# Kernel tuning notes

Hardware: AMD Instinct MI355X
Metric: run time of the kernel (lower is better)

The kernel has to match this reference:

```python
import jax, jax.numpy as jnp
import numpy as np

D_MODEL = 1024
NUM_HEADS = 16
D_K = D_MODEL // NUM_HEADS
B, S = 4, 2048


def setup_inputs() -> dict:
    key = jax.random.key(0)
    k1, k2, k3 = jax.random.split(key, 3)
    x = jax.random.normal(k1, (B, S, D_MODEL), dtype=jnp.float32)
    w_qkv = jax.random.normal(k2, (3, NUM_HEADS, D_K, D_MODEL), dtype=jnp.float32) / np.sqrt(D_MODEL)
    w_o = jax.random.normal(k3, (D_MODEL, D_MODEL), dtype=jnp.float32) / np.sqrt(D_MODEL)
    return {"x": x, "w_qkv": w_qkv, "w_o": w_o}


def reference(x, w_qkv, w_o):
    # x: [b, s, m]; w_qkv: [3, h, k, m]; w_o: [m, m]
    seq_len = x.shape[-2]
    d_k = w_qkv.shape[-2]
    # fused QKV projection for all heads: [3, b, h, s, k]
    qkv = jnp.einsum('bsm,qhkm->qbhsk', x, w_qkv)
    Q, K, V = qkv[0], qkv[1], qkv[2]
    # attention scores [b, h, s, s]
    scores = jnp.einsum('bhsk,bhtk->bhst', Q, K) / jnp.sqrt(jnp.asarray(d_k, x.dtype))
    # causal mask: position t > s is masked
    causal = jnp.tril(jnp.ones((seq_len, seq_len), dtype=bool))
    scores = jnp.where(causal, scores, -jnp.inf)
    probs = jax.nn.softmax(scores, axis=-1)
    # attn_pdrop = 0.0 -> dropout is identity
    attn = jnp.einsum('bhst,bhtk->bhsk', probs, V)
    # concat heads: [b, s, h*k]
    b, h, s, k = attn.shape
    attn_cat = jnp.transpose(attn, (0, 2, 1, 3)).reshape(b, s, h * k)
    # output projection: y = attn_cat @ w_o^T
    return jnp.einsum('bsd,md->bsm', attn_cat, w_o)
```

## Files before the change

### kernel.cpp

```cpp
#include <hip/hip_runtime.h>
#include <hip/hip_bf16.h>


#define D_MODEL 1024
#define NUM_HEADS 16
#define D_KD 64
#define B_SZ 4
#define S_LEN 2048
#define ROWS (B_SZ * S_LEN)
#define QKV_N (3 * D_MODEL)

typedef __attribute__((ext_vector_type(8))) short short8;
typedef __attribute__((ext_vector_type(4))) float f32x4;
typedef __attribute__((ext_vector_type(16))) float f32x16;

__device__ __forceinline__ unsigned f2bf(float f) {
    unsigned u = __builtin_bit_cast(unsigned, f);
    return (u + 0x7FFFu + ((u >> 16) & 1u)) >> 16;
}
__device__ __forceinline__ uint2 pack_bf16x4(float4 v) {
    uint2 u;
    u.x = f2bf(v.x) | (f2bf(v.y) << 16);
    u.y = f2bf(v.z) | (f2bf(v.w) << 16);
    return u;
}

template <int MODE>
__global__ __launch_bounds__(256) void gemm_bt_mfma(const float* __restrict__ A,
                                                    const float* __restrict__ Bm,
                                                    float* __restrict__ C,
                                                    int M, int N, int K) {
    __shared__ unsigned short As[128][40];
    __shared__ unsigned short Bs[128][40];

    const int t = threadIdx.x;
    const int lane = t & 63;
    const int w = t >> 6;
    const int wr = w >> 1, wc = w & 1;
    const int row0 = blockIdx.y * 128;
    const int col0 = blockIdx.x * 128;

    const int srow = t >> 3;
    const int skc = (t & 7) << 2;

    const float* Abase = A + (size_t)row0 * K;
    const float* Bbase = Bm + (size_t)col0 * K;

    f32x4 acc[4][4];
#pragma unroll
    for (int m = 0; m < 4; ++m)
#pragma unroll
        for (int n = 0; n < 4; ++n)
#pragma unroll
            for (int j = 0; j < 4; ++j) acc[m][n][j] = 0.f;

    float4 pa[4], pb[4];
    const int q8 = (lane >> 4) << 3;
    const int frA = wr * 64 + (lane & 15);
    const int frB = wc * 64 + (lane & 15);
    const int NT = K >> 5;

#pragma unroll
    for (int i = 0; i < 4; ++i) {
        int r = i * 32 + srow;
        pa[i] = *reinterpret_cast<const float4*>(&Abase[(size_t)r * K + skc]);
        pb[i] = *reinterpret_cast<const float4*>(&Bbase[(size_t)r * K + skc]);
    }

    for (int kt = 0; kt < NT; ++kt) {
        __syncthreads();
#pragma unroll
        for (int i = 0; i < 4; ++i) {
            int r = i * 32 + srow;
            *reinterpret_cast<uint2*>(&As[r][skc]) = pack_bf16x4(pa[i]);
            *reinterpret_cast<uint2*>(&Bs[r][skc]) = pack_bf16x4(pb[i]);
        }
        __syncthreads();

        if (kt + 1 < NT) {
            const int k0n = (kt + 1) << 5;
#pragma unroll
            for (int i = 0; i < 4; ++i) {
                int r = i * 32 + srow;
                pa[i] = *reinterpret_cast<const float4*>(&Abase[(size_t)r * K + k0n + skc]);
                pb[i] = *reinterpret_cast<const float4*>(&Bbase[(size_t)r * K + k0n + skc]);
            }
        }

        short8 afr[4], bfr[4];
#pragma unroll
        for (int m = 0; m < 4; ++m)
            afr[m] = *reinterpret_cast<const short8*>(&As[frA + m * 16][q8]);
#pragma unroll
        for (int n = 0; n < 4; ++n)
            bfr[n] = *reinterpret_cast<const short8*>(&Bs[frB + n * 16][q8]);
#pragma unroll
        for (int m = 0; m < 4; ++m)
#pragma unroll
            for (int n = 0; n < 4; ++n)
                acc[m][n] = __builtin_amdgcn_mfma_f32_16x16x32_bf16(afr[m], bfr[n],
                                                                    acc[m][n], 0, 0, 0);
    }

    const int orow = row0 + wr * 64 + ((lane >> 4) << 2);
    const int ocol = col0 + wc * 64 + (lane & 15);
#pragma unroll
    for (int m = 0; m < 4; ++m)
#pragma unroll
        for (int n = 0; n < 4; ++n) {
            const int cg = ocol + n * 16;
#pragma unroll
            for (int j = 0; j < 4; ++j) {
                const int rg = orow + m * 16 + j;
                const float v = acc[m][n][j];
                if (MODE == 0) {
                    int q = cg >> 10, h = (cg >> 6) & 15, kk = cg & 63;
                    int b = rg >> 11, s = rg & 2047;
                    C[((((size_t)q * B_SZ + b) * NUM_HEADS + h) * S_LEN + s) * D_KD + kk] = v;
                } else {
                    C[(size_t)rg * N + cg] = v;
                }
            }
        }
}

__global__ __launch_bounds__(512, 2) void flash_attn_mfma_v2(const float* __restrict__ qkv,
                                                             float* __restrict__ attn_out) {
    const int qb = (int)gridDim.x - 1 - (int)blockIdx.x;
    const int h = blockIdx.y;
    const int b = blockIdx.z;
    const int t = threadIdx.x;
    const int lane = t & 63;
    const int w = t >> 6;
    const int l31 = lane & 31;
    const int hi = lane >> 5;

    __shared__ unsigned short smem[256 * 72];
    __shared__ float fbuf[8][32];

    unsigned short* Qs = smem;
    unsigned short* Ks = smem;
    unsigned short* Vt = smem + 64 * 72;

    const size_t head_elems = (size_t)S_LEN * D_KD;
    const float* Qg = qkv + (((size_t)0 * B_SZ + b) * NUM_HEADS + h) * head_elems;
    const float* Kg = qkv + (((size_t)1 * B_SZ + b) * NUM_HEADS + h) * head_elems;
    const float* Vg = qkv + (((size_t)2 * B_SZ + b) * NUM_HEADS + h) * head_elems;

    const int q0 = qb * 256;
    const int qmin = q0 + 32 * w;

#pragma unroll
    for (int lx = 0; lx < 8; ++lx) {
        int idx = t + lx * 512;
        int r = idx >> 4;
        int c = (idx & 15) << 2;
        float4 v = *reinterpret_cast<const float4*>(&Qg[(size_t)(q0 + r) * D_KD + c]);
        v.x *= 0.125f; v.y *= 0.125f; v.z *= 0.125f; v.w *= 0.125f;
        *reinterpret_cast<uint2*>(&Qs[r * 72 + c]) = pack_bf16x4(v);
    }
    __syncthreads();

    short8 qfr[4];
#pragma unroll
    for (int ks = 0; ks < 4; ++ks)
        qfr[ks] = *reinterpret_cast<const short8*>(&Qs[(32 * w + l31) * 72 + 16 * ks + 8 * hi]);

    f32x16 oacc[2];
#pragma unroll
    for (int n = 0; n < 2; ++n)
#pragma unroll
        for (int j = 0; j < 16; ++j) oacc[n][j] = 0.f;
    float m = -1e30f, lsum = 0.f;

    const int nt = 4 * (qb + 1);
    for (int tt = 0; tt < nt; ++tt) {
        const int c0 = tt * 64;
        __syncthreads();

        if (w < 4) {
#pragma unroll
            for (int lx = 0; lx < 4; ++lx) {
                int idx = t + lx * 256;
                int r = idx >> 4;
                int c = (idx & 15) << 2;
                float4 v = *reinterpret_cast<const float4*>(&Kg[(size_t)(c0 + r) * D_KD + c]);
                *reinterpret_cast<uint2*>(&Ks[r * 72 + c]) = pack_bf16x4(v);
            }
        } else {
            int t2 = t - 256;
            int tb = (t2 >> 4) << 2;
            int dk0 = (t2 & 15) << 2;
            float4 vv[4];
#pragma unroll
            for (int i = 0; i < 4; ++i)
                vv[i] = *reinterpret_cast<const float4*>(&Vg[(size_t)(c0 + tb + i) * D_KD + dk0]);
            const float* vp = reinterpret_cast<const float*>(&vv[0]);
#pragma unroll
            for (int j = 0; j < 4; ++j) {
                uint2 u;
                u.x = f2bf(vp[0 * 4 + j]) | (f2bf(vp[1 * 4 + j]) << 16);
                u.y = f2bf(vp[2 * 4 + j]) | (f2bf(vp[3 * 4 + j]) << 16);
                *reinterpret_cast<uint2*>(&Vt[(dk0 + j) * 72 + tb]) = u;
            }
        }
        __syncthreads();

        for (int st = 0; st < 2; ++st) {
            const int t0s = c0 + 32 * st;
            if (t0s > qmin) break;
            const bool diag = (t0s == qmin);

            f32x16 s;
#pragma unroll
            for (int j = 0; j < 16; ++j) s[j] = 0.f;
#pragma unroll
            for (int ks = 0; ks < 4; ++ks) {
                short8 ka = *reinterpret_cast<const short8*>(
                    &Ks[(32 * st + l31) * 72 + 16 * ks + 8 * hi]);
                s = __builtin_amdgcn_mfma_f32_32x32x16_bf16(ka, qfr[ks], s, 0, 0, 0);
            }
            if (diag) {
#pragma unroll
                for (int reg = 0; reg < 16; ++reg) {
                    const int tloc = (reg & 3) + 8 * (reg >> 2) + 4 * hi;
                    if (tloc > l31) s[reg] = -1e30f;
                }
            }

            float pm = s[0];
#pragma unroll
            for (int reg = 1; reg < 16; ++reg) pm = fmaxf(pm, s[reg]);
            pm = fmaxf(pm, __shfl_xor(pm, 32));

            if (!__all(pm <= m + 8.0f)) {
                const float mnew = fmaxf(m, pm);
                const float al = __expf(m - mnew);
                m = mnew;
                lsum *= al;
                fbuf[w][l31] = al;
#pragma unroll
                for (int g = 0; g < 4; ++g) {
                    float4 a4 = *reinterpret_cast<float4*>(&fbuf[w][8 * g + 4 * hi]);
                    const float* ap = reinterpret_cast<const float*>(&a4);
#pragma unroll
                    for (int j = 0; j < 4; ++j) {
                        oacc[0][4 * g + j] *= ap[j];
                        oacc[1][4 * g + j] *= ap[j];
                    }
                }
            }

            float p[16];
            float ps = 0.f;
#pragma unroll
            for (int reg = 0; reg < 16; ++reg) {
                p[reg] = __expf(s[reg] - m);
                ps += p[reg];
            }
            ps += __shfl_xor(ps, 32);
            lsum += ps;

            unsigned pk[8], sw[8];
#pragma unroll
            for (int i = 0; i < 8; ++i) pk[i] = f2bf(p[2 * i]) | (f2bf(p[2 * i + 1]) << 16);
#pragma unroll
            for (int i = 0; i < 8; ++i) sw[i] = (unsigned)__shfl_xor((int)pk[i], 32);

            union { unsigned u[4]; short8 s8; } a0, a1;
            a0.u[0] = hi ? sw[2] : pk[0];
            a0.u[1] = hi ? sw[3] : pk[1];
            a0.u[2] = hi ? pk[2] : sw[0];
            a0.u[3] = hi ? pk[3] : sw[1];
            a1.u[0] = hi ? sw[6] : pk[4];
            a1.u[1] = hi ? sw[7] : pk[5];
            a1.u[2] = hi ? pk[6] : sw[4];
            a1.u[3] = hi ? pk[7] : sw[5];

#pragma unroll
            for (int n = 0; n < 2; ++n) {
                const unsigned short* vrow = &Vt[(32 * n + l31) * 72 + 32 * st + 8 * hi];
                short8 vb0 = *reinterpret_cast<const short8*>(vrow);
                short8 vb1 = *reinterpret_cast<const short8*>(vrow + 16);
                oacc[n] = __builtin_amdgcn_mfma_f32_32x32x16_bf16(a0.s8, vb0, oacc[n], 0, 0, 0);
                oacc[n] = __builtin_amdgcn_mfma_f32_32x32x16_bf16(a1.s8, vb1, oacc[n], 0, 0, 0);
            }
        }
    }

    const float inv = 1.f / lsum;
    fbuf[w][l31] = inv;
#pragma unroll
    for (int g = 0; g < 4; ++g) {
        float4 i4 = *reinterpret_cast<float4*>(&fbuf[w][8 * g + 4 * hi]);
        const float* ip = reinterpret_cast<const float*>(&i4);
#pragma unroll
        for (int j = 0; j < 4; ++j) {
            const int reg = 4 * g + j;
            const int qrow = q0 + 32 * w + 8 * g + 4 * hi + j;
            const size_t base = ((size_t)(b * S_LEN + qrow)) * D_MODEL + h * D_KD + l31;
            attn_out[base] = oacc[0][reg] * ip[j];
            attn_out[base + 32] = oacc[1][reg] * ip[j];
        }
    }
}

extern "C" void kernel_launch(void* const* d_in, const int* in_sizes, int n_in,
                              void* d_out, int out_size, void* d_ws, size_t ws_size,
                              hipStream_t stream) {
    const float* x = (const float*)d_in[0];
    const float* w_qkv = (const float*)d_in[1];
    const float* w_o = (const float*)d_in[2];
    float* out = (float*)d_out;

    float* qkv = (float*)d_ws;
    float* attn = qkv + (size_t)3 * B_SZ * NUM_HEADS * S_LEN * D_KD;

    gemm_bt_mfma<0><<<dim3(QKV_N / 128, ROWS / 128), dim3(256), 0, stream>>>(
        x, w_qkv, qkv, ROWS, QKV_N, D_MODEL);
    flash_attn_mfma_v2<<<dim3(S_LEN / 256, NUM_HEADS, B_SZ), dim3(512), 0, stream>>>(qkv, attn);
    gemm_bt_mfma<1><<<dim3(D_MODEL / 128, ROWS / 128), dim3(256), 0, stream>>>(
        attn, w_o, out, ROWS, D_MODEL, D_MODEL);
}
```

Baseline: 364.3 us.

## Switch pipeline to bf16 intermediates with pre-converted inputs and direct-to-LDS GEMM loads

Three small kernels first convert x, w_qkv and w_o to bf16. The QKV GEMM then writes bf16 Q/K/V, with the 1/sqrt(d_k) scale folded into its epilogue, and attention writes a bf16 attention output. This halves intermediate traffic and removes per-tile float-to-bf16 conversion inside the attention and GEMM loops. The GEMM now loads tiles with global_load_lds into unpadded shared memory, which drops the register prefetch overlap and may add LDS bank conflicts. The attention MFMA sections are also wrapped in s_setprio to favour matrix issue.

```diff
diff --git a/kernel.cpp b/kernel.cpp
--- a/kernel.cpp
+++ b/kernel.cpp
@@ -13,6 +13,7 @@
 typedef __attribute__((ext_vector_type(8))) short short8;
 typedef __attribute__((ext_vector_type(4))) float f32x4;
 typedef __attribute__((ext_vector_type(16))) float f32x16;
+typedef unsigned short ushort_t;
 
 __device__ __forceinline__ unsigned f2bf(float f) {
     unsigned u = __builtin_bit_cast(unsigned, f);
@@ -24,14 +25,30 @@
     u.y = f2bf(v.z) | (f2bf(v.w) << 16);
     return u;
 }
+__device__ __forceinline__ void gload16(void* lds, const void* g) {
+    __builtin_amdgcn_global_load_lds(
+        (const __attribute__((address_space(1))) unsigned int*)(g),
+        (__attribute__((address_space(3))) unsigned int*)(lds), 16, 0, 0);
+}
+
+__global__ __launch_bounds__(256) void cvt_bf16(const float* __restrict__ src,
+                                                ushort_t* __restrict__ dst, int n4) {
+    int i = blockIdx.x * blockDim.x + threadIdx.x;
+    const int stride = gridDim.x * blockDim.x;
+    for (; i < n4; i += stride) {
+        float4 v = reinterpret_cast<const float4*>(src)[i];
+        *reinterpret_cast<uint2*>(&dst[(size_t)i * 4]) = pack_bf16x4(v);
+    }
+}
 
 template <int MODE>
-__global__ __launch_bounds__(256) void gemm_bt_mfma(const float* __restrict__ A,
-                                                    const float* __restrict__ Bm,
-                                                    float* __restrict__ C,
+__global__ __launch_bounds__(256) void gemm_bt_bf16(const ushort_t* __restrict__ A,
+                                                    const ushort_t* __restrict__ Bm,
+                                                    ushort_t* __restrict__ Cb,
+                                                    float* __restrict__ Cf,
                                                     int M, int N, int K) {
-    __shared__ unsigned short As[128][40];
-    __shared__ unsigned short Bs[128][40];
+    __shared__ ushort_t As[128 * 32];
+    __shared__ ushort_t Bs[128 * 32];
 
     const int t = threadIdx.x;
     const int lane = t & 63;
@@ -40,11 +57,15 @@
     const int row0 = blockIdx.y * 128;
     const int col0 = blockIdx.x * 128;
 
-    const int srow = t >> 3;
-    const int skc = (t & 7) << 2;
-
-    const float* Abase = A + (size_t)row0 * K;
-    const float* Bbase = Bm + (size_t)col0 * K;
+    const int srow = t >> 2;
+    const int sk8 = (t & 3) << 3;
+
+    const ushort_t* Ag = A + (size_t)(row0 + srow) * K + sk8;
+    const ushort_t* Bg = Bm + (size_t)(col0 + srow) * K + sk8;
+    ushort_t* ldsA0 = &As[(size_t)t * 8];
+    ushort_t* ldsA1 = &As[(size_t)(t + 256) * 8];
+    ushort_t* ldsB0 = &Bs[(size_t)t * 8];
+    ushort_t* ldsB1 = &Bs[(size_t)(t + 256) * 8];
 
     f32x4 acc[4][4];
 #pragma unroll
@@ -54,46 +75,27 @@
 #pragma unroll
             for (int j = 0; j < 4; ++j) acc[m][n][j] = 0.f;
 
-    float4 pa[4], pb[4];
     const int q8 = (lane >> 4) << 3;
     const int frA = wr * 64 + (lane & 15);
     const int frB = wc * 64 + (lane & 15);
     const int NT = K >> 5;
 
-#pragma unroll
-    for (int i = 0; i < 4; ++i) {
-        int r = i * 32 + srow;
-        pa[i] = *reinterpret_cast<const float4*>(&Abase[(size_t)r * K + skc]);
-        pb[i] = *reinterpret_cast<const float4*>(&Bbase[(size_t)r * K + skc]);
-    }
-
     for (int kt = 0; kt < NT; ++kt) {
+        const int k0 = kt << 5;
         __syncthreads();
-#pragma unroll
-        for (int i = 0; i < 4; ++i) {
-            int r = i * 32 + srow;
-            *reinterpret_cast<uint2*>(&As[r][skc]) = pack_bf16x4(pa[i]);
-            *reinterpret_cast<uint2*>(&Bs[r][skc]) = pack_bf16x4(pb[i]);
-        }
+        gload16(ldsA0, Ag + k0);
+        gload16(ldsA1, Ag + (size_t)64 * K + k0);
+        gload16(ldsB0, Bg + k0);
+        gload16(ldsB1, Bg + (size_t)64 * K + k0);
         __syncthreads();
 
-        if (kt + 1 < NT) {
-            const int k0n = (kt + 1) << 5;
-#pragma unroll
-            for (int i = 0; i < 4; ++i) {
-                int r = i * 32 + srow;
-                pa[i] = *reinterpret_cast<const float4*>(&Abase[(size_t)r * K + k0n + skc]);
-                pb[i] = *reinterpret_cast<const float4*>(&Bbase[(size_t)r * K + k0n + skc]);
-            }
-        }
-
         short8 afr[4], bfr[4];
 #pragma unroll
         for (int m = 0; m < 4; ++m)
-            afr[m] = *reinterpret_cast<const short8*>(&As[frA + m * 16][q8]);
+            afr[m] = *reinterpret_cast<const short8*>(&As[(frA + m * 16) * 32 + q8]);
 #pragma unroll
         for (int n = 0; n < 4; ++n)
-            bfr[n] = *reinterpret_cast<const short8*>(&Bs[frB + n * 16][q8]);
+            bfr[n] = *reinterpret_cast<const short8*>(&Bs[(frB + n * 16) * 32 + q8]);
 #pragma unroll
         for (int m = 0; m < 4; ++m)
 #pragma unroll
@@ -112,20 +114,22 @@
 #pragma unroll
             for (int j = 0; j < 4; ++j) {
                 const int rg = orow + m * 16 + j;
-                const float v = acc[m][n][j];
+                float v = acc[m][n][j];
                 if (MODE == 0) {
-                    int q = cg >> 10, h = (cg >> 6) & 15, kk = cg & 63;
-                    int b = rg >> 11, s = rg & 2047;
-                    C[((((size_t)q * B_SZ + b) * NUM_HEADS + h) * S_LEN + s) * D_KD + kk] = v;
+                    const int q = cg >> 10, hh = (cg >> 6) & 15, kk = cg & 63;
+                    const int bb = rg >> 11, s = rg & 2047;
+                    if (q == 0) v *= 0.125f;
+                    Cb[((((size_t)q * B_SZ + bb) * NUM_HEADS + hh) * S_LEN + s) * D_KD + kk] =
+                        (ushort_t)f2bf(v);
                 } else {
-                    C[(size_t)rg * N + cg] = v;
+                    Cf[(size_t)rg * N + cg] = v;
                 }
             }
         }
 }
 
-__global__ __launch_bounds__(512, 2) void flash_attn_mfma_v2(const float* __restrict__ qkv,
-                                                             float* __restrict__ attn_out) {
+__global__ __launch_bounds__(512, 2) void flash_attn_mfma_v3(const ushort_t* __restrict__ qkv,
+                                                             ushort_t* __restrict__ attn_out) {
     const int qb = (int)gridDim.x - 1 - (int)blockIdx.x;
     const int h = blockIdx.y;
     const int b = blockIdx.z;
@@ -135,29 +139,27 @@
     const int l31 = lane & 31;
     const int hi = lane >> 5;
 
-    __shared__ unsigned short smem[256 * 72];
+    __shared__ ushort_t smem[256 * 72];
     __shared__ float fbuf[8][32];
-
-    unsigned short* Qs = smem;
-    unsigned short* Ks = smem;
-    unsigned short* Vt = smem + 64 * 72;
+    ushort_t* Qs = smem;
+    ushort_t* Ks = smem;
+    ushort_t* Vt = smem + 64 * 72;
 
     const size_t head_elems = (size_t)S_LEN * D_KD;
-    const float* Qg = qkv + (((size_t)0 * B_SZ + b) * NUM_HEADS + h) * head_elems;
-    const float* Kg = qkv + (((size_t)1 * B_SZ + b) * NUM_HEADS + h) * head_elems;
-    const float* Vg = qkv + (((size_t)2 * B_SZ + b) * NUM_HEADS + h) * head_elems;
+    const ushort_t* Qg = qkv + (((size_t)0 * B_SZ + b) * NUM_HEADS + h) * head_elems;
+    const ushort_t* Kg = qkv + (((size_t)1 * B_SZ + b) * NUM_HEADS + h) * head_elems;
+    const ushort_t* Vg = qkv + (((size_t)2 * B_SZ + b) * NUM_HEADS + h) * head_elems;
 
     const int q0 = qb * 256;
     const int qmin = q0 + 32 * w;
 
 #pragma unroll
-    for (int lx = 0; lx < 8; ++lx) {
+    for (int lx = 0; lx < 4; ++lx) {
         int idx = t + lx * 512;
-        int r = idx >> 4;
-        int c = (idx & 15) << 2;
-        float4 v = *reinterpret_cast<const float4*>(&Qg[(size_t)(q0 + r) * D_KD + c]);
-        v.x *= 0.125f; v.y *= 0.125f; v.z *= 0.125f; v.w *= 0.125f;
-        *reinterpret_cast<uint2*>(&Qs[r * 72 + c]) = pack_bf16x4(v);
+        int r = idx >> 3;
+        int c8 = (idx & 7) << 3;
+        *reinterpret_cast<uint4*>(&Qs[r * 72 + c8]) =
+            *reinterpret_cast<const uint4*>(&Qg[(size_t)(q0 + r) * D_KD + c8]);
     }
     __syncthreads();
 
@@ -180,28 +182,25 @@
 
         if (w < 4) {
 #pragma unroll
-            for (int lx = 0; lx < 4; ++lx) {
-                int idx = t + lx * 256;
-                int r = idx >> 4;
-                int c = (idx & 15) << 2;
-                float4 v = *reinterpret_cast<const float4*>(&Kg[(size_t)(c0 + r) * D_KD + c]);
-                *reinterpret_cast<uint2*>(&Ks[r * 72 + c]) = pack_bf16x4(v);
+            for (int i = 0; i < 2; ++i) {
+                int j = t + i * 256;
+                int r = j >> 3;
+                int c8 = (j & 7) << 3;
+                *reinterpret_cast<uint4*>(&Ks[r * 72 + c8]) =
+                    *reinterpret_cast<const uint4*>(&Kg[(size_t)(c0 + r) * D_KD + c8]);
             }
         } else {
             int t2 = t - 256;
-            int tb = (t2 >> 4) << 2;
-            int dk0 = (t2 & 15) << 2;
-            float4 vv[4];
-#pragma unroll
-            for (int i = 0; i < 4; ++i)
-                vv[i] = *reinterpret_cast<const float4*>(&Vg[(size_t)(c0 + tb + i) * D_KD + dk0]);
-            const float* vp = reinterpret_cast<const float*>(&vv[0]);
-#pragma unroll
-            for (int j = 0; j < 4; ++j) {
-                uint2 u;
-                u.x = f2bf(vp[0 * 4 + j]) | (f2bf(vp[1 * 4 + j]) << 16);
-                u.y = f2bf(vp[2 * 4 + j]) | (f2bf(vp[3 * 4 + j]) << 16);
-                *reinterpret_cast<uint2*>(&Vt[(dk0 + j) * 72 + tb]) = u;
+            int tp = t2 & 31, dg = t2 >> 5;
+            int t0 = tp * 2, d0 = dg * 8;
+            uint4 va = *reinterpret_cast<const uint4*>(&Vg[(size_t)(c0 + t0) * D_KD + d0]);
+            uint4 vb = *reinterpret_cast<const uint4*>(&Vg[(size_t)(c0 + t0 + 1) * D_KD + d0]);
+            const ushort_t* ua = reinterpret_cast<const ushort_t*>(&va);
+            const ushort_t* ub = reinterpret_cast<const ushort_t*>(&vb);
+#pragma unroll
+            for (int d = 0; d < 8; ++d) {
+                unsigned u = (unsigned)ua[d] | ((unsigned)ub[d] << 16);
+                *reinterpret_cast<unsigned*>(&Vt[(d0 + d) * 72 + t0]) = u;
             }
         }
         __syncthreads();
@@ -214,12 +213,14 @@
             f32x16 s;
 #pragma unroll
             for (int j = 0; j < 16; ++j) s[j] = 0.f;
+            __builtin_amdgcn_s_setprio(1);
 #pragma unroll
             for (int ks = 0; ks < 4; ++ks) {
                 short8 ka = *reinterpret_cast<const short8*>(
                     &Ks[(32 * st + l31) * 72 + 16 * ks + 8 * hi]);
                 s = __builtin_amdgcn_mfma_f32_32x32x16_bf16(ka, qfr[ks], s, 0, 0, 0);
             }
+            __builtin_amdgcn_s_setprio(0);
             if (diag) {
 #pragma unroll
                 for (int reg = 0; reg < 16; ++reg) {
@@ -277,14 +278,16 @@
             a1.u[2] = hi ? pk[6] : sw[4];
             a1.u[3] = hi ? pk[7] : sw[5];
 
+            __builtin_amdgcn_s_setprio(1);
 #pragma unroll
             for (int n = 0; n < 2; ++n) {
-                const unsigned short* vrow = &Vt[(32 * n + l31) * 72 + 32 * st + 8 * hi];
+                const ushort_t* vrow = &Vt[(32 * n + l31) * 72 + 32 * st + 8 * hi];
                 short8 vb0 = *reinterpret_cast<const short8*>(vrow);
                 short8 vb1 = *reinterpret_cast<const short8*>(vrow + 16);
                 oacc[n] = __builtin_amdgcn_mfma_f32_32x32x16_bf16(a0.s8, vb0, oacc[n], 0, 0, 0);
                 oacc[n] = __builtin_amdgcn_mfma_f32_32x32x16_bf16(a1.s8, vb1, oacc[n], 0, 0, 0);
             }
+            __builtin_amdgcn_s_setprio(0);
         }
     }
 
@@ -299,8 +302,8 @@
             const int reg = 4 * g + j;
             const int qrow = q0 + 32 * w + 8 * g + 4 * hi + j;
             const size_t base = ((size_t)(b * S_LEN + qrow)) * D_MODEL + h * D_KD + l31;
-            attn_out[base] = oacc[0][reg] * ip[j];
-            attn_out[base + 32] = oacc[1][reg] * ip[j];
+            attn_out[base] = (ushort_t)f2bf(oacc[0][reg] * ip[j]);
+            attn_out[base + 32] = (ushort_t)f2bf(oacc[1][reg] * ip[j]);
         }
     }
 }
@@ -313,12 +316,19 @@
     const float* w_o = (const float*)d_in[2];
     float* out = (float*)d_out;
 
-    float* qkv = (float*)d_ws;
-    float* attn = qkv + (size_t)3 * B_SZ * NUM_HEADS * S_LEN * D_KD;
-
-    gemm_bt_mfma<0><<<dim3(QKV_N / 128, ROWS / 128), dim3(256), 0, stream>>>(
-        x, w_qkv, qkv, ROWS, QKV_N, D_MODEL);
-    flash_attn_mfma_v2<<<dim3(S_LEN / 256, NUM_HEADS, B_SZ), dim3(512), 0, stream>>>(qkv, attn);
-    gemm_bt_mfma<1><<<dim3(D_MODEL / 128, ROWS / 128), dim3(256), 0, stream>>>(
-        attn, w_o, out, ROWS, D_MODEL, D_MODEL);
-}
+    ushort_t* xb = (ushort_t*)d_ws;
+    ushort_t* wqb = xb + 8388608;
+    ushort_t* wob = wqb + 3145728;
+    ushort_t* qkvb = wob + 1048576;
+    ushort_t* attnb = qkvb + 25165824;
+
+    cvt_bf16<<<2048, 256, 0, stream>>>(x, xb, 8388608 / 4);
+    cvt_bf16<<<1024, 256, 0, stream>>>(w_qkv, wqb, 3145728 / 4);
+    cvt_bf16<<<512, 256, 0, stream>>>(w_o, wob, 1048576 / 4);
+
+    gemm_bt_bf16<0><<<dim3(QKV_N / 128, ROWS / 128), dim3(256), 0, stream>>>(
+        xb, wqb, qkvb, nullptr, ROWS, QKV_N, D_MODEL);
+    flash_attn_mfma_v3<<<dim3(S_LEN / 256, NUM_HEADS, B_SZ), dim3(512), 0, stream>>>(qkvb, attnb);
+    gemm_bt_bf16<1><<<dim3(D_MODEL / 128, ROWS / 128), dim3(256), 0, stream>>>(
+        attnb, wob, nullptr, out, ROWS, D_MODEL, D_MODEL);
+}
```

After: 311.7 us. 1.17x faster.
